# Kernel optimization log

Measured on AMD Instinct MI355X. Metric: run time of the kernel, lower is better.

The kernel has to match this reference:

```python
import jax, jax.numpy as jnp
import numpy as np

N_AGENTS = 262144
GRID = 1024
C = 8
HIDDEN = 64
DT = 0.1
SENSOR_ANGLE = 0.6
SENSOR_LEN = 3.0
DECAY = 0.99


def setup_inputs() -> dict:
    key = jax.random.key(0)
    k1, k2, k3, k4, k5 = jax.random.split(key, 5)
    agent_pos = jax.random.uniform(k1, (2, N_AGENTS), minval=2.0, maxval=GRID - 2.0, dtype=jnp.float32)
    agent_vel = jax.random.uniform(k2, (2, N_AGENTS), minval=-1.0, maxval=1.0, dtype=jnp.float32)
    pheremone_lattice = jax.random.uniform(k3, (C, GRID, GRID), dtype=jnp.float32)
    W1 = jax.random.normal(k4, (3 * C, HIDDEN), dtype=jnp.float32) * 0.1
    b1 = jnp.zeros((HIDDEN,), dtype=jnp.float32)
    W2 = jax.random.normal(k5, (HIDDEN, 2 + C), dtype=jnp.float32) * 0.1
    b2 = jnp.zeros((2 + C,), dtype=jnp.float32)
    return {"agent_pos": agent_pos, "agent_vel": agent_vel, "pheremone_lattice": pheremone_lattice,
            "W1": W1, "b1": b1, "W2": W2, "b2": b2}


def _sense(agent_pos, agent_vel, lattice):
    # heading angle per agent, 3 sensor offsets: 0, +a, -a
    theta = jnp.arctan2(agent_vel[1], agent_vel[0])                      # [N]
    offs = jnp.array([0.0, SENSOR_ANGLE, -SENSOR_ANGLE], dtype=agent_pos.dtype)
    ang = theta[None, :] + offs[:, None]                                  # [3,N]
    cx = jnp.rint(agent_pos[0][None, :] + SENSOR_LEN * jnp.cos(ang)).astype(jnp.int32)  # [3,N]
    cy = jnp.rint(agent_pos[1][None, :] + SENSOR_LEN * jnp.sin(ang)).astype(jnp.int32)
    d = jnp.array([-1, 0, 1], dtype=jnp.int32)
    xi = (cx[:, :, None] + d) % GRID                                      # [3,N,3]
    yi = (cy[:, :, None] + d) % GRID
    # Cartesian product of x and y offsets (meshgrid in original) -> 3x3 window
    X = xi[:, :, :, None]                                                 # [3,N,3,1]
    Y = yi[:, :, None, :]                                                 # [3,N,1,3]
    vals = lattice[:, X, Y]                                               # [C,3,N,3,3]
    w = vals.sum(axis=(-1, -2))                                           # [C,3,N]
    return w[:, 0].T, w[:, 1].T, w[:, 2].T                                # each [N,C]


def reference(agent_pos, agent_vel, pheremone_lattice, W1, b1, W2, b2):
    w_front, w_left, w_right = _sense(agent_pos, agent_vel, pheremone_lattice)
    # per-agent MLP (vmapped agent_nn in original): concat 3 sensor readings
    x = jnp.concatenate([w_front, w_left, w_right], axis=-1)              # [N,3C]
    h = jnp.tanh(x @ W1 + b1)                                             # [N,HIDDEN]
    o = h @ W2 + b2                                                       # [N,2+C]
    new_vel = o[:, :2].T                                                  # [2,N]
    d_pher = o[:, 2:].T                                                   # [C,N]
    # deposit pheremones at rounded agent positions (scatter-set, relu clamp)
    pos_i = jnp.rint(agent_pos).astype(jnp.int32)                         # [2,N]
    cur = pheremone_lattice[:, pos_i[0], pos_i[1]]                        # [C,N]
    lat = pheremone_lattice.at[:, pos_i[0], pos_i[1]].set(jax.nn.relu(cur + DT * d_pher))
    # gaussian_blur == 0 -> diffusion is identity; then decay
    lat = lat * DECAY
    # periodic position update
    new_pos = (agent_pos + new_vel * DT) % GRID
    return (new_pos, new_vel, lat)
```

## Files before the change

### kernel.cpp

```cpp
#include <hip/hip_runtime.h>
#include <hip/hip_bf16.h>
#include <math.h>

#define GRIDN 1024
#define NAGENTS 262144
#define CCH 8
#define HIDDEN 64
#define DT 0.1f
#define DECAYF 0.99f
#define SENSOR_LEN 3.0f
#define COS_SA 0.82533561490967829724f
#define SIN_SA 0.56464247339503535720f

typedef __attribute__((ext_vector_type(8))) short short8;
typedef __attribute__((ext_vector_type(2))) _Float16 half2v;

__device__ __forceinline__ float dot2f(unsigned a, unsigned b, float c) {
#if __has_builtin(__builtin_amdgcn_fdot2)
    return __builtin_amdgcn_fdot2(__builtin_bit_cast(half2v, a),
                                  __builtin_bit_cast(half2v, b), c, false);
#else
    half2v ha = __builtin_bit_cast(half2v, a), hb = __builtin_bit_cast(half2v, b);
    return c + (float)ha.x * (float)hb.x + (float)ha.y * (float)hb.y;
#endif
}

__device__ __forceinline__ unsigned packh(float a, float b) {
    _Float16 ha = (_Float16)a, hb = (_Float16)b;
    unsigned short ua = __builtin_bit_cast(unsigned short, ha);
    unsigned short ub = __builtin_bit_cast(unsigned short, hb);
    return (unsigned)ua | ((unsigned)ub << 16);
}

__device__ __forceinline__ float fast_tanh(float x) {
    float xc = fminf(fmaxf(x, -9.0f), 9.0f);
    float t = __builtin_amdgcn_exp2f(xc * 2.88539008177792681472f);
    return (t - 1.0f) * __builtin_amdgcn_rcpf(t + 1.0f);
}

__global__ void __launch_bounds__(256) k_boxT(const float* __restrict__ lat,
                                              _Float16* __restrict__ BT,
                                              int* __restrict__ winner,
                                              const float* __restrict__ W1,
                                              const float* __restrict__ W2,
                                              unsigned* __restrict__ W1p,
                                              unsigned* __restrict__ W2p) {
    if (blockIdx.x == 0) {
        for (int t = threadIdx.x; t < 768 + 512; t += 256) {
            if (t < 768) {
                int p = t >> 6, j = t & 63;
                W1p[t] = packh(W1[(2 * p) * HIDDEN + j], W1[(2 * p + 1) * HIDDEN + j]);
            } else {
                int q = t - 768;
                int pg = q >> 4, k = q & 15;
                unsigned v = 0;
                if (k < 10) v = packh(W2[(2 * pg) * 10 + k], W2[(2 * pg + 1) * 10 + k]);
                W2p[q] = v;
            }
        }
    }
    int idx = blockIdx.x * blockDim.x + threadIdx.x;
    winner[idx] = -1;
    int x = idx >> 10, y = idx & (GRIDN - 1);
    int xm = (x + GRIDN - 1) & (GRIDN - 1), xp = (x + 1) & (GRIDN - 1);
    int ym = (y + GRIDN - 1) & (GRIDN - 1), yp = (y + 1) & (GRIDN - 1);
    _Float16 out[CCH];
#pragma unroll
    for (int c = 0; c < CCH; ++c) {
        const float* L = lat + (size_t)c * GRIDN * GRIDN;
        const float* r0 = L + xm * GRIDN;
        const float* r1 = L + x * GRIDN;
        const float* r2 = L + xp * GRIDN;
        float s = r0[ym] + r0[y] + r0[yp]
                + r1[ym] + r1[y] + r1[yp]
                + r2[ym] + r2[y] + r2[yp];
        out[c] = (_Float16)s;
    }
    *(short8*)(BT + (size_t)idx * CCH) = *(const short8*)out;
}

__global__ void __launch_bounds__(256) k_agent(
    const float* __restrict__ pos, const float* __restrict__ vel,
    const _Float16* __restrict__ BT,
    const unsigned* __restrict__ W1p, const float* __restrict__ b1,
    const unsigned* __restrict__ W2p, const float* __restrict__ b2,
    float* __restrict__ out_pos, float* __restrict__ out_vel,
    float* __restrict__ dp, int* __restrict__ winner) {
    __shared__ float part[4][64][13];

    int lane = threadIdx.x & 63;
    int wq = __builtin_amdgcn_readfirstlane(threadIdx.x >> 6);
    int i = blockIdx.x * 64 + lane;

    float px = pos[i], py = pos[i + NAGENTS];
    float vx = vel[i], vy = vel[i + NAGENTS];

    float r2 = vx * vx + vy * vy;
    float ct, st;
    if (r2 > 0.f) {
        float inv = rsqrtf(r2);
        ct = vx * inv;
        st = vy * inv;
    } else {
        ct = 1.f;
        st = 0.f;
    }

    float dirx[3], diry[3];
    dirx[0] = ct;                          diry[0] = st;
    dirx[1] = ct * COS_SA - st * SIN_SA;   diry[1] = st * COS_SA + ct * SIN_SA;
    dirx[2] = ct * COS_SA + st * SIN_SA;   diry[2] = st * COS_SA - ct * SIN_SA;

    uint4 raw[3];
#pragma unroll
    for (int s = 0; s < 3; ++s) {
        int gx = ((int)rintf(px + SENSOR_LEN * dirx[s]) + GRIDN) & (GRIDN - 1);
        int gy = ((int)rintf(py + SENSOR_LEN * diry[s]) + GRIDN) & (GRIDN - 1);
        raw[s] = *(const uint4*)(BT + ((size_t)(gx << 10) + gy) * CCH);
    }
    unsigned xk[12];
#pragma unroll
    for (int s = 0; s < 3; ++s) {
        xk[s * 4 + 0] = raw[s].x; xk[s * 4 + 1] = raw[s].y;
        xk[s * 4 + 2] = raw[s].z; xk[s * 4 + 3] = raw[s].w;
    }

    float h[16];
    {
        const float4* b1v = (const float4*)(b1 + wq * 16);
#pragma unroll
        for (int q = 0; q < 4; ++q) {
            float4 b = b1v[q];
            h[q * 4 + 0] = b.x; h[q * 4 + 1] = b.y;
            h[q * 4 + 2] = b.z; h[q * 4 + 3] = b.w;
        }
    }
#pragma unroll
    for (int p = 0; p < 12; ++p) {
        unsigned xp = xk[p];
        const unsigned* wrow = W1p + p * HIDDEN + wq * 16;
#pragma unroll
        for (int jj = 0; jj < 16; ++jj) h[jj] = dot2f(xp, wrow[jj], h[jj]);
    }

    unsigned hp[8];
#pragma unroll
    for (int p = 0; p < 8; ++p)
        hp[p] = packh(fast_tanh(h[2 * p]), fast_tanh(h[2 * p + 1]));

    float o[2 + CCH];
#pragma unroll
    for (int k = 0; k < 2 + CCH; ++k) o[k] = 0.f;
#pragma unroll
    for (int p = 0; p < 8; ++p) {
        const unsigned* w2row = W2p + (wq * 8 + p) * 16;
#pragma unroll
        for (int k = 0; k < 2 + CCH; ++k) o[k] = dot2f(hp[p], w2row[k], o[k]);
    }

#pragma unroll
    for (int k = 0; k < 2 + CCH; ++k) part[wq][lane][k] = o[k];
    __syncthreads();

    if (wq == 0) {
        float s0 = part[0][lane][0] + part[1][lane][0] + part[2][lane][0] + part[3][lane][0] + b2[0];
        float s1 = part[0][lane][1] + part[1][lane][1] + part[2][lane][1] + part[3][lane][1] + b2[1];
        float npx = px + s0 * DT;
        if (npx >= (float)GRIDN) npx -= (float)GRIDN;
        if (npx < 0.f) npx += (float)GRIDN;
        float npy = py + s1 * DT;
        if (npy >= (float)GRIDN) npy -= (float)GRIDN;
        if (npy < 0.f) npy += (float)GRIDN;
        out_pos[i] = npx;
        out_pos[i + NAGENTS] = npy;
        out_vel[i] = s0;
        out_vel[i + NAGENTS] = s1;
    } else if (wq == 1) {
        float d0 = part[0][lane][2] + part[1][lane][2] + part[2][lane][2] + part[3][lane][2] + b2[2];
        float d1 = part[0][lane][3] + part[1][lane][3] + part[2][lane][3] + part[3][lane][3] + b2[3];
        float d2 = part[0][lane][4] + part[1][lane][4] + part[2][lane][4] + part[3][lane][4] + b2[4];
        float d3 = part[0][lane][5] + part[1][lane][5] + part[2][lane][5] + part[3][lane][5] + b2[5];
        *(float4*)(dp + (size_t)i * CCH) = make_float4(d0, d1, d2, d3);
    } else if (wq == 2) {
        float d4 = part[0][lane][6] + part[1][lane][6] + part[2][lane][6] + part[3][lane][6] + b2[6];
        float d5 = part[0][lane][7] + part[1][lane][7] + part[2][lane][7] + part[3][lane][7] + b2[7];
        float d6 = part[0][lane][8] + part[1][lane][8] + part[2][lane][8] + part[3][lane][8] + b2[8];
        float d7 = part[0][lane][9] + part[1][lane][9] + part[2][lane][9] + part[3][lane][9] + b2[9];
        *(float4*)(dp + (size_t)i * CCH + 4) = make_float4(d4, d5, d6, d7);
    } else {
        int wx = (int)rintf(px) & (GRIDN - 1);
        int wy = (int)rintf(py) & (GRIDN - 1);
        atomicMax(&winner[(wx << 10) + wy], i);
    }
}

__global__ void __launch_bounds__(256) k_update(const float* __restrict__ lat,
                                                const int* __restrict__ winner,
                                                const float* __restrict__ dp,
                                                float* __restrict__ out_lat) {
    int idx = blockIdx.x * blockDim.x + threadIdx.x;
    int w = winner[idx];
    float d[CCH];
    if (w >= 0) {
        const float4* dpp = (const float4*)(dp + (size_t)w * CCH);
        float4 a = dpp[0], b = dpp[1];
        d[0] = a.x; d[1] = a.y; d[2] = a.z; d[3] = a.w;
        d[4] = b.x; d[5] = b.y; d[6] = b.z; d[7] = b.w;
    }
#pragma unroll
    for (int c = 0; c < CCH; ++c) {
        size_t off = (size_t)c * GRIDN * GRIDN + idx;
        float v = lat[off];
        if (w >= 0) v = fmaxf(v + DT * d[c], 0.f);
        out_lat[off] = v * DECAYF;
    }
}

extern "C" void kernel_launch(void* const* d_in, const int* in_sizes, int n_in,
                              void* d_out, int out_size, void* d_ws, size_t ws_size,
                              hipStream_t stream) {
    const float* pos = (const float*)d_in[0];
    const float* vel = (const float*)d_in[1];
    const float* lat = (const float*)d_in[2];
    const float* W1  = (const float*)d_in[3];
    const float* b1  = (const float*)d_in[4];
    const float* W2  = (const float*)d_in[5];
    const float* b2  = (const float*)d_in[6];

    float* out      = (float*)d_out;
    float* out_pos  = out;
    float* out_vel  = out + 2 * NAGENTS;
    float* out_lat  = out + 4 * NAGENTS;

    char* ws = (char*)d_ws;
    int*       winner = (int*)ws;
    float*     dp     = (float*)(ws + (4 << 20));
    _Float16*  BT     = (_Float16*)(ws + (12 << 20));
    unsigned*  W1p    = (unsigned*)(ws + (28 << 20));
    unsigned*  W2p    = (unsigned*)(ws + (28 << 20) + 4096);

    const int ncell = GRIDN * GRIDN;

    k_boxT<<<ncell / 256, 256, 0, stream>>>(lat, BT, winner, W1, W2, W1p, W2p);
    k_agent<<<NAGENTS / 64, 256, 0, stream>>>(pos, vel, BT, W1p, b1, W2p, b2,
                                              out_pos, out_vel, dp, winner);
    k_update<<<ncell / 256, 256, 0, stream>>>(lat, winner, dp, out_lat);
}
```

Before: 60.59 us.

## Compute two rows per thread in box-sum and split sensor gathers across waves

The box-sum kernel now has each thread produce two adjacent output rows, so the shared middle row sums are reused and row loads drop from six to four per pair of cells; the grid is halved to match. In the agent kernel, each of three waves gathers one sensor's box-sum vector and writes it to shared memory, while the fourth wave does the winner atomicMax early. After a barrier all waves read the full sensor input from LDS. This spreads the latency of the random gathers across waves instead of having every wave issue all three redundantly, at the cost of an extra barrier and LDS traffic.

After: 63.42 us. +4.7%, slower.

```diff
diff --git a/kernel.cpp b/kernel.cpp
--- a/kernel.cpp
+++ b/kernel.cpp
@@ -59,24 +59,35 @@
             }
         }
     }
-    int idx = blockIdx.x * blockDim.x + threadIdx.x;
-    winner[idx] = -1;
-    int x = idx >> 10, y = idx & (GRIDN - 1);
-    int xm = (x + GRIDN - 1) & (GRIDN - 1), xp = (x + 1) & (GRIDN - 1);
+    int b = blockIdx.x;
+    int x = (b >> 2) * 2;
+    int y = (b & 3) * 256 + threadIdx.x;
+    int idx0 = (x << 10) + y;
+    int idx1 = idx0 + GRIDN;
+    winner[idx0] = -1;
+    winner[idx1] = -1;
+
+    int xm = (x + GRIDN - 1) & (GRIDN - 1);
+    int xp2 = (x + 2) & (GRIDN - 1);
     int ym = (y + GRIDN - 1) & (GRIDN - 1), yp = (y + 1) & (GRIDN - 1);
-    _Float16 out[CCH];
+
+    _Float16 out0[CCH], out1[CCH];
 #pragma unroll
     for (int c = 0; c < CCH; ++c) {
         const float* L = lat + (size_t)c * GRIDN * GRIDN;
-        const float* r0 = L + xm * GRIDN;
-        const float* r1 = L + x * GRIDN;
-        const float* r2 = L + xp * GRIDN;
-        float s = r0[ym] + r0[y] + r0[yp]
-                + r1[ym] + r1[y] + r1[yp]
-                + r2[ym] + r2[y] + r2[yp];
-        out[c] = (_Float16)s;
-    }
-    *(short8*)(BT + (size_t)idx * CCH) = *(const short8*)out;
+        const float* ra = L + xm * GRIDN;
+        const float* rb = L + x * GRIDN;
+        const float* rc = L + (x + 1) * GRIDN;
+        const float* rd = L + xp2 * GRIDN;
+        float sa = ra[ym] + ra[y] + ra[yp];
+        float sb = rb[ym] + rb[y] + rb[yp];
+        float sc = rc[ym] + rc[y] + rc[yp];
+        float sd = rd[ym] + rd[y] + rd[yp];
+        out0[c] = (_Float16)(sa + sb + sc);
+        out1[c] = (_Float16)(sb + sc + sd);
+    }
+    *(short8*)(BT + (size_t)idx0 * CCH) = *(const short8*)out0;
+    *(short8*)(BT + (size_t)idx1 * CCH) = *(const short8*)out1;
 }
 
 __global__ void __launch_bounds__(256) k_agent(
@@ -86,6 +97,7 @@
     const unsigned* __restrict__ W2p, const float* __restrict__ b2,
     float* __restrict__ out_pos, float* __restrict__ out_vel,
     float* __restrict__ dp, int* __restrict__ winner) {
+    __shared__ unsigned sens[12][64];
     __shared__ float part[4][64][13];
 
     int lane = threadIdx.x & 63;
@@ -93,37 +105,41 @@
     int i = blockIdx.x * 64 + lane;
 
     float px = pos[i], py = pos[i + NAGENTS];
-    float vx = vel[i], vy = vel[i + NAGENTS];
-
-    float r2 = vx * vx + vy * vy;
-    float ct, st;
-    if (r2 > 0.f) {
-        float inv = rsqrtf(r2);
-        ct = vx * inv;
-        st = vy * inv;
+
+    if (wq < 3) {
+        float vx = vel[i], vy = vel[i + NAGENTS];
+        float r2 = vx * vx + vy * vy;
+        float ct, st;
+        if (r2 > 0.f) {
+            float inv = rsqrtf(r2);
+            ct = vx * inv;
+            st = vy * inv;
+        } else {
+            ct = 1.f;
+            st = 0.f;
+        }
+        float dx, dy;
+        if (wq == 0)      { dx = ct;                        dy = st; }
+        else if (wq == 1) { dx = ct * COS_SA - st * SIN_SA; dy = st * COS_SA + ct * SIN_SA; }
+        else              { dx = ct * COS_SA + st * SIN_SA; dy = st * COS_SA - ct * SIN_SA; }
+
+        int gx = ((int)rintf(px + SENSOR_LEN * dx) + GRIDN) & (GRIDN - 1);
+        int gy = ((int)rintf(py + SENSOR_LEN * dy) + GRIDN) & (GRIDN - 1);
+        uint4 u = *(const uint4*)(BT + ((size_t)(gx << 10) + gy) * CCH);
+        sens[wq * 4 + 0][lane] = u.x;
+        sens[wq * 4 + 1][lane] = u.y;
+        sens[wq * 4 + 2][lane] = u.z;
+        sens[wq * 4 + 3][lane] = u.w;
     } else {
-        ct = 1.f;
-        st = 0.f;
-    }
-
-    float dirx[3], diry[3];
-    dirx[0] = ct;                          diry[0] = st;
-    dirx[1] = ct * COS_SA - st * SIN_SA;   diry[1] = st * COS_SA + ct * SIN_SA;
-    dirx[2] = ct * COS_SA + st * SIN_SA;   diry[2] = st * COS_SA - ct * SIN_SA;
-
-    uint4 raw[3];
-#pragma unroll
-    for (int s = 0; s < 3; ++s) {
-        int gx = ((int)rintf(px + SENSOR_LEN * dirx[s]) + GRIDN) & (GRIDN - 1);
-        int gy = ((int)rintf(py + SENSOR_LEN * diry[s]) + GRIDN) & (GRIDN - 1);
-        raw[s] = *(const uint4*)(BT + ((size_t)(gx << 10) + gy) * CCH);
-    }
+        int wx = (int)rintf(px) & (GRIDN - 1);
+        int wy = (int)rintf(py) & (GRIDN - 1);
+        atomicMax(&winner[(wx << 10) + wy], i);
+    }
+    __syncthreads();
+
     unsigned xk[12];
 #pragma unroll
-    for (int s = 0; s < 3; ++s) {
-        xk[s * 4 + 0] = raw[s].x; xk[s * 4 + 1] = raw[s].y;
-        xk[s * 4 + 2] = raw[s].z; xk[s * 4 + 3] = raw[s].w;
-    }
+    for (int p = 0; p < 12; ++p) xk[p] = sens[p][lane];
 
     float h[16];
     {
@@ -187,10 +203,6 @@
         float d6 = part[0][lane][8] + part[1][lane][8] + part[2][lane][8] + part[3][lane][8] + b2[8];
         float d7 = part[0][lane][9] + part[1][lane][9] + part[2][lane][9] + part[3][lane][9] + b2[9];
         *(float4*)(dp + (size_t)i * CCH + 4) = make_float4(d4, d5, d6, d7);
-    } else {
-        int wx = (int)rintf(px) & (GRIDN - 1);
-        int wy = (int)rintf(py) & (GRIDN - 1);
-        atomicMax(&winner[(wx << 10) + wy], i);
     }
 }
 
@@ -241,7 +253,7 @@
 
     const int ncell = GRIDN * GRIDN;
 
-    k_boxT<<<ncell / 256, 256, 0, stream>>>(lat, BT, winner, W1, W2, W1p, W2p);
+    k_boxT<<<ncell / 2 / 256, 256, 0, stream>>>(lat, BT, winner, W1, W2, W1p, W2p);
     k_agent<<<NAGENTS / 64, 256, 0, stream>>>(pos, vel, BT, W1p, b1, W2p, b2,
                                               out_pos, out_vel, dp, winner);
     k_update<<<ncell / 256, 256, 0, stream>>>(lat, winner, dp, out_lat);
```

## Split agent kernel into sense and per-thread MLP kernels

Applied to the files above, without the earlier changes.

Splits the fused agent kernel into two. k_sense gathers the three box-filtered sensor samples into a 12.6MB workspace buffer and does the winner atomicMax. k_mlp then runs the whole 64-wide hidden layer in one thread per agent. This removes the four-wave split of the hidden layer, along with its shared-memory reduction and __syncthreads, and quadruples the agents handled per block. In exchange it adds a kernel launch, an extra global write and read of the sensor data, and much higher register pressure from 64 hidden accumulators.

Measured after the change: 86.19 us. 42.2% more time.

```diff
diff --git a/kernel.cpp b/kernel.cpp
--- a/kernel.cpp
+++ b/kernel.cpp
@@ -1,5 +1,4 @@
 #include <hip/hip_runtime.h>
-#include <hip/hip_bf16.h>
 #include <math.h>
 
 #define GRIDN 1024
@@ -79,19 +78,12 @@
     *(short8*)(BT + (size_t)idx * CCH) = *(const short8*)out;
 }
 
-__global__ void __launch_bounds__(256) k_agent(
-    const float* __restrict__ pos, const float* __restrict__ vel,
-    const _Float16* __restrict__ BT,
-    const unsigned* __restrict__ W1p, const float* __restrict__ b1,
-    const unsigned* __restrict__ W2p, const float* __restrict__ b2,
-    float* __restrict__ out_pos, float* __restrict__ out_vel,
-    float* __restrict__ dp, int* __restrict__ winner) {
-    __shared__ float part[4][64][13];
-
-    int lane = threadIdx.x & 63;
-    int wq = __builtin_amdgcn_readfirstlane(threadIdx.x >> 6);
-    int i = blockIdx.x * 64 + lane;
-
+__global__ void __launch_bounds__(256) k_sense(const float* __restrict__ pos,
+                                               const float* __restrict__ vel,
+                                               const _Float16* __restrict__ BT,
+                                               uint4* __restrict__ XK,
+                                               int* __restrict__ winner) {
+    int i = blockIdx.x * blockDim.x + threadIdx.x;
     float px = pos[i], py = pos[i + NAGENTS];
     float vx = vel[i], vy = vel[i + NAGENTS];
 
@@ -111,87 +103,73 @@
     dirx[1] = ct * COS_SA - st * SIN_SA;   diry[1] = st * COS_SA + ct * SIN_SA;
     dirx[2] = ct * COS_SA + st * SIN_SA;   diry[2] = st * COS_SA - ct * SIN_SA;
 
-    uint4 raw[3];
 #pragma unroll
     for (int s = 0; s < 3; ++s) {
         int gx = ((int)rintf(px + SENSOR_LEN * dirx[s]) + GRIDN) & (GRIDN - 1);
         int gy = ((int)rintf(py + SENSOR_LEN * diry[s]) + GRIDN) & (GRIDN - 1);
-        raw[s] = *(const uint4*)(BT + ((size_t)(gx << 10) + gy) * CCH);
-    }
-    unsigned xk[12];
-#pragma unroll
-    for (int s = 0; s < 3; ++s) {
-        xk[s * 4 + 0] = raw[s].x; xk[s * 4 + 1] = raw[s].y;
-        xk[s * 4 + 2] = raw[s].z; xk[s * 4 + 3] = raw[s].w;
-    }
-
-    float h[16];
-    {
-        const float4* b1v = (const float4*)(b1 + wq * 16);
-#pragma unroll
-        for (int q = 0; q < 4; ++q) {
-            float4 b = b1v[q];
-            h[q * 4 + 0] = b.x; h[q * 4 + 1] = b.y;
-            h[q * 4 + 2] = b.z; h[q * 4 + 3] = b.w;
-        }
-    }
+        XK[(size_t)i * 3 + s] = *(const uint4*)(BT + ((size_t)(gx << 10) + gy) * CCH);
+    }
+
+    int wx = (int)rintf(px) & (GRIDN - 1);
+    int wy = (int)rintf(py) & (GRIDN - 1);
+    atomicMax(&winner[(wx << 10) + wy], i);
+}
+
+__global__ void __launch_bounds__(256) k_mlp(
+    const float* __restrict__ pos,
+    const uint4* __restrict__ XK,
+    const unsigned* __restrict__ W1p, const float* __restrict__ b1,
+    const unsigned* __restrict__ W2p, const float* __restrict__ b2,
+    float* __restrict__ out_pos, float* __restrict__ out_vel,
+    float* __restrict__ dp) {
+    int i = blockIdx.x * blockDim.x + threadIdx.x;
+
+    uint4 g0 = XK[(size_t)i * 3 + 0];
+    uint4 g1 = XK[(size_t)i * 3 + 1];
+    uint4 g2 = XK[(size_t)i * 3 + 2];
+    unsigned xk[12] = {g0.x, g0.y, g0.z, g0.w,
+                       g1.x, g1.y, g1.z, g1.w,
+                       g2.x, g2.y, g2.z, g2.w};
+
+    float h[HIDDEN];
+#pragma unroll
+    for (int j = 0; j < HIDDEN; ++j) h[j] = b1[j];
 #pragma unroll
     for (int p = 0; p < 12; ++p) {
         unsigned xp = xk[p];
-        const unsigned* wrow = W1p + p * HIDDEN + wq * 16;
-#pragma unroll
-        for (int jj = 0; jj < 16; ++jj) h[jj] = dot2f(xp, wrow[jj], h[jj]);
-    }
-
-    unsigned hp[8];
-#pragma unroll
-    for (int p = 0; p < 8; ++p)
-        hp[p] = packh(fast_tanh(h[2 * p]), fast_tanh(h[2 * p + 1]));
+        const unsigned* wrow = W1p + p * HIDDEN;
+#pragma unroll
+        for (int j = 0; j < HIDDEN; ++j) h[j] = dot2f(xp, wrow[j], h[j]);
+    }
 
     float o[2 + CCH];
 #pragma unroll
-    for (int k = 0; k < 2 + CCH; ++k) o[k] = 0.f;
-#pragma unroll
-    for (int p = 0; p < 8; ++p) {
-        const unsigned* w2row = W2p + (wq * 8 + p) * 16;
-#pragma unroll
-        for (int k = 0; k < 2 + CCH; ++k) o[k] = dot2f(hp[p], w2row[k], o[k]);
-    }
-
-#pragma unroll
-    for (int k = 0; k < 2 + CCH; ++k) part[wq][lane][k] = o[k];
-    __syncthreads();
-
-    if (wq == 0) {
-        float s0 = part[0][lane][0] + part[1][lane][0] + part[2][lane][0] + part[3][lane][0] + b2[0];
-        float s1 = part[0][lane][1] + part[1][lane][1] + part[2][lane][1] + part[3][lane][1] + b2[1];
-        float npx = px + s0 * DT;
-        if (npx >= (float)GRIDN) npx -= (float)GRIDN;
-        if (npx < 0.f) npx += (float)GRIDN;
-        float npy = py + s1 * DT;
-        if (npy >= (float)GRIDN) npy -= (float)GRIDN;
-        if (npy < 0.f) npy += (float)GRIDN;
-        out_pos[i] = npx;
-        out_pos[i + NAGENTS] = npy;
-        out_vel[i] = s0;
-        out_vel[i + NAGENTS] = s1;
-    } else if (wq == 1) {
-        float d0 = part[0][lane][2] + part[1][lane][2] + part[2][lane][2] + part[3][lane][2] + b2[2];
-        float d1 = part[0][lane][3] + part[1][lane][3] + part[2][lane][3] + part[3][lane][3] + b2[3];
-        float d2 = part[0][lane][4] + part[1][lane][4] + part[2][lane][4] + part[3][lane][4] + b2[4];
-        float d3 = part[0][lane][5] + part[1][lane][5] + part[2][lane][5] + part[3][lane][5] + b2[5];
-        *(float4*)(dp + (size_t)i * CCH) = make_float4(d0, d1, d2, d3);
-    } else if (wq == 2) {
-        float d4 = part[0][lane][6] + part[1][lane][6] + part[2][lane][6] + part[3][lane][6] + b2[6];
-        float d5 = part[0][lane][7] + part[1][lane][7] + part[2][lane][7] + part[3][lane][7] + b2[7];
-        float d6 = part[0][lane][8] + part[1][lane][8] + part[2][lane][8] + part[3][lane][8] + b2[8];
-        float d7 = part[0][lane][9] + part[1][lane][9] + part[2][lane][9] + part[3][lane][9] + b2[9];
-        *(float4*)(dp + (size_t)i * CCH + 4) = make_float4(d4, d5, d6, d7);
-    } else {
-        int wx = (int)rintf(px) & (GRIDN - 1);
-        int wy = (int)rintf(py) & (GRIDN - 1);
-        atomicMax(&winner[(wx << 10) + wy], i);
-    }
+    for (int k = 0; k < 2 + CCH; ++k) o[k] = b2[k];
+#pragma unroll
+    for (int p = 0; p < 32; ++p) {
+        unsigned hp = packh(fast_tanh(h[2 * p]), fast_tanh(h[2 * p + 1]));
+        const unsigned* w2row = W2p + p * 16;
+#pragma unroll
+        for (int k = 0; k < 2 + CCH; ++k) o[k] = dot2f(hp, w2row[k], o[k]);
+    }
+
+    float px = pos[i], py = pos[i + NAGENTS];
+    float nvx = o[0], nvy = o[1];
+    float npx = px + nvx * DT;
+    if (npx >= (float)GRIDN) npx -= (float)GRIDN;
+    if (npx < 0.f) npx += (float)GRIDN;
+    float npy = py + nvy * DT;
+    if (npy >= (float)GRIDN) npy -= (float)GRIDN;
+    if (npy < 0.f) npy += (float)GRIDN;
+
+    out_pos[i] = npx;
+    out_pos[i + NAGENTS] = npy;
+    out_vel[i] = nvx;
+    out_vel[i + NAGENTS] = nvy;
+
+    float4* dpp = (float4*)(dp + (size_t)i * CCH);
+    dpp[0] = make_float4(o[2], o[3], o[4], o[5]);
+    dpp[1] = make_float4(o[6], o[7], o[8], o[9]);
 }
 
 __global__ void __launch_bounds__(256) k_update(const float* __restrict__ lat,
@@ -238,11 +216,13 @@
     _Float16*  BT     = (_Float16*)(ws + (12 << 20));
     unsigned*  W1p    = (unsigned*)(ws + (28 << 20));
     unsigned*  W2p    = (unsigned*)(ws + (28 << 20) + 4096);
+    uint4*     XK     = (uint4*)(ws + (29 << 20));
 
     const int ncell = GRIDN * GRIDN;
 
     k_boxT<<<ncell / 256, 256, 0, stream>>>(lat, BT, winner, W1, W2, W1p, W2p);
-    k_agent<<<NAGENTS / 64, 256, 0, stream>>>(pos, vel, BT, W1p, b1, W2p, b2,
-                                              out_pos, out_vel, dp, winner);
+    k_sense<<<NAGENTS / 256, 256, 0, stream>>>(pos, vel, BT, XK, winner);
+    k_mlp<<<NAGENTS / 256, 256, 0, stream>>>(pos, XK, W1p, b1, W2p, b2,
+                                             out_pos, out_vel, dp);
     k_update<<<ncell / 256, 256, 0, stream>>>(lat, winner, dp, out_lat);
 }
```
